# Optimization experiments

Hardware: AMD Instinct MI355X
Metric: run time of the kernel (lower is better)

The kernel has to match this reference:

```python
import jax, jax.numpy as jnp
import numpy as np

D_MODEL = 256
MLP_DIM = 1024
EPS = 1e-5

def _layernorm(x, g, b):
    mu = jnp.mean(x, axis=-1, keepdims=True)
    var = jnp.mean(jnp.square(x - mu), axis=-1, keepdims=True)
    return (x - mu) * jax.lax.rsqrt(var + EPS) * g + b

def setup_inputs() -> dict:
    key = jax.random.key(0)
    ks = jax.random.split(key, 4)
    d, m = D_MODEL, MLP_DIM
    x = jax.random.normal(ks[0], (8, 1024, 4, d), dtype=jnp.float32)
    w_qkv = jax.random.normal(ks[1], (3 * d, d), dtype=jnp.float32) * 0.05  # torch Linear weight (out,in)
    gamma1 = jnp.ones((d,), jnp.float32)
    beta1 = jnp.zeros((d,), jnp.float32)
    gamma2 = jnp.ones((d,), jnp.float32)
    beta2 = jnp.zeros((d,), jnp.float32)
    w1 = jax.random.normal(ks[2], (m, d), dtype=jnp.float32) * 0.05
    b1 = jnp.zeros((m,), jnp.float32)
    w2 = jax.random.normal(ks[3], (d, m), dtype=jnp.float32) * 0.05
    b2 = jnp.zeros((d,), jnp.float32)
    return {"x": x, "w_qkv": w_qkv, "gamma1": gamma1, "beta1": beta1,
            "gamma2": gamma2, "beta2": beta2, "w1": w1, "b1": b1, "w2": w2, "b2": b2}

def reference(x, w_qkv, gamma1, beta1, gamma2, beta2, w1, b1, w2, b2):
    bsz, n, h, d = x.shape
    scale = d ** -0.5
    # --- attention branch: x + attn(norm1(x)) ---
    xn = _layernorm(x, gamma1, beta1)
    # Linear(d, 3d): xn @ W^T, then reshape trailing 3d -> (d, 3) as in torch
    qkv = jnp.einsum('bnhd,ed->bnhe', xn, w_qkv).reshape(bsz, n * h, d, 3)
    q, k, v = qkv[..., 0], qkv[..., 1], qkv[..., 2]   # [b, n*h, d]
    dots = jnp.einsum('bid,bjd->bij', q, k) * scale   # [b, n*h, n*h]
    attn = jax.nn.softmax(dots, axis=-1)              # dropout=0 -> identity
    out = jnp.einsum('bij,bjd->bid', attn, v).reshape(bsz, n, h, d)
    x = x + out
    # --- mlp branch: x + mlp(norm2(x)) ---
    xn2 = _layernorm(x, gamma2, beta2)
    hid = jax.nn.silu(jnp.einsum('bnhd,md->bnhm', xn2, w1) + b1)
    x = x + jnp.einsum('bnhm,dm->bnhd', hid, w2) + b2
    return x
```

## Files before the change

kernel.cpp:

```cpp
#include <hip/hip_runtime.h>


typedef __attribute__((ext_vector_type(8))) short bf16x8;
typedef __attribute__((ext_vector_type(4))) short bf16x4;
typedef __attribute__((ext_vector_type(4))) float f32x4;
typedef __attribute__((ext_vector_type(16))) float f32x16;

static __device__ __forceinline__ short f2bf(float f) {
    union { float f; unsigned u; } v; v.f = f;
    unsigned r = (v.u + 0x7FFFu + ((v.u >> 16) & 1u)) >> 16;
    return (short)r;
}

static __device__ __forceinline__ void gll16(const void* g, void* l) {
    __builtin_amdgcn_global_load_lds(
        (const __attribute__((address_space(1))) unsigned*)g,
        (__attribute__((address_space(3))) unsigned*)l, 16, 0, 0);
}

__global__ __launch_bounds__(256) void k_cvt(const float* __restrict__ wqkv,
                                             const float* __restrict__ w1,
                                             const float* __restrict__ w2,
                                             short* __restrict__ owqkv,
                                             short* __restrict__ ow1,
                                             short* __restrict__ ow2) {
    int i = blockIdx.x * 256 + threadIdx.x;
    if (i < 196608) {
        int e = i >> 8, col = i & 255;
        int dd = e / 3, which = e - dd * 3;
        float v = wqkv[i];
        if (which == 0) v *= 0.0625f * 1.44269504f;
        owqkv[((which << 8) + dd) * 256 + col] = f2bf(v);
    }
    if (i < 262144) { ow1[i] = f2bf(w1[i]); ow2[i] = f2bf(w2[i]); }
}

__global__ __launch_bounds__(256) void k_ln(const float* __restrict__ x,
                                            const float* __restrict__ g,
                                            const float* __restrict__ bta,
                                            short* __restrict__ out) {
    int w = threadIdx.x >> 6, lane = threadIdx.x & 63;
    long row = (long)blockIdx.x * 4 + w;
    float4 v = *((const float4*)(x + row * 256) + lane);
    float s = v.x + v.y + v.z + v.w;
    float q = v.x * v.x + v.y * v.y + v.z * v.z + v.w * v.w;
    for (int off = 1; off < 64; off <<= 1) {
        s += __shfl_xor(s, off);
        q += __shfl_xor(q, off);
    }
    float mean = s * (1.0f / 256.0f);
    float var = q * (1.0f / 256.0f) - mean * mean;
    float rstd = rsqrtf(var + 1e-5f);
    float4 gg = *((const float4*)g + lane);
    float4 bb = *((const float4*)bta + lane);
    short4 o;
    o.x = f2bf((v.x - mean) * rstd * gg.x + bb.x);
    o.y = f2bf((v.y - mean) * rstd * gg.y + bb.y);
    o.z = f2bf((v.z - mean) * rstd * gg.z + bb.z);
    o.w = f2bf((v.w - mean) * rstd * gg.w + bb.w);
    *((short4*)(out + row * 256) + lane) = o;
}

__global__ __launch_bounds__(256) void k_qkv(const short* __restrict__ xn,
                                             const short* __restrict__ wb,
                                             short* __restrict__ Q,
                                             short* __restrict__ K,
                                             short* __restrict__ VT) {
    __shared__ __attribute__((aligned(16))) short lds_a[64 * 264];
    __shared__ __attribute__((aligned(16))) short lds_b[64 * 264];
    int t = threadIdx.x;
    int m0 = blockIdx.y * 64, n0 = blockIdx.x * 64;
    const int4* ga = (const int4*)xn;
    const int4* gb = (const int4*)wb;
    int4* la = (int4*)lds_a;
    int4* lb = (int4*)lds_b;
    for (int it = 0; it < 8; it++) {
        int c = t + 256 * it;
        int r = c >> 5, k = c & 31;
        la[r * 33 + k] = ga[(long)(m0 + r) * 32 + k];
        lb[r * 33 + k] = gb[(n0 + r) * 32 + k];
    }
    __syncthreads();
    int w = t >> 6, lane = t & 63, ln = lane & 15, qd = lane >> 4;
    int moff = (w >> 1) * 32, noff = (w & 1) * 32;
    f32x4 acc[2][2] = {};
    for (int ks = 0; ks < 8; ks++) {
        bf16x8 a0 = *(const bf16x8*)&lds_a[(moff + ln) * 264 + ks * 32 + qd * 8];
        bf16x8 a1 = *(const bf16x8*)&lds_a[(moff + 16 + ln) * 264 + ks * 32 + qd * 8];
        bf16x8 b0 = *(const bf16x8*)&lds_b[(noff + ln) * 264 + ks * 32 + qd * 8];
        bf16x8 b1 = *(const bf16x8*)&lds_b[(noff + 16 + ln) * 264 + ks * 32 + qd * 8];
        acc[0][0] = __builtin_amdgcn_mfma_f32_16x16x32_bf16(a0, b0, acc[0][0], 0, 0, 0);
        acc[0][1] = __builtin_amdgcn_mfma_f32_16x16x32_bf16(a0, b1, acc[0][1], 0, 0, 0);
        acc[1][0] = __builtin_amdgcn_mfma_f32_16x16x32_bf16(a1, b0, acc[1][0], 0, 0, 0);
        acc[1][1] = __builtin_amdgcn_mfma_f32_16x16x32_bf16(a1, b1, acc[1][1], 0, 0, 0);
    }
    for (int mi = 0; mi < 2; mi++)
        for (int nj = 0; nj < 2; nj++)
            for (int rg = 0; rg < 4; rg++) {
                float v = acc[mi][nj][rg];
                int gr = m0 + moff + mi * 16 + qd * 4 + rg;
                int e = n0 + noff + nj * 16 + ln;
                int which = e >> 8, dd = e & 255;
                short bv = f2bf(v);
                if (which == 0) Q[(long)gr * 256 + dd] = bv;
                else if (which == 1) K[(long)gr * 256 + dd] = bv;
                else {
                    int b = gr >> 12, i = gr & 4095;
                    VT[((long)b * 256 + dd) * 4096 + i] = bv;
                }
            }
}

__global__ __launch_bounds__(512, 2) void k_attn(const short* __restrict__ Q,
                                                 const short* __restrict__ K,
                                                 const short* __restrict__ VT,
                                                 const float* __restrict__ x,
                                                 float* __restrict__ out) {
    __shared__ __attribute__((aligned(16))) short lds_k[2][64 * 256];
    __shared__ __attribute__((aligned(16))) short lds_v[2][2][256 * 40];
    int t = threadIdx.x, w = t >> 6, l = t & 63, l5 = l & 31, h = l >> 5;
    int ww = w & 3, hkv = w >> 2;
    int b = blockIdx.x;
    int q0 = blockIdx.y * 128 + ww * 32;

    bf16x8 qf[16];
    {
        const short* qrow = Q + ((long)(b * 4096 + q0 + l5)) * 256;
        #pragma unroll
        for (int kc = 0; kc < 16; kc++) qf[kc] = *(const bf16x8*)(qrow + kc * 16 + h * 8);
    }
    f32x16 O[8] = {};
    float lsum = 0.f;

    const char* Kb = (const char*)(K + (long)b * 4096 * 256);
    const int4* gv = (const int4*)(VT + (long)b * 4096 * 256);

    int koff[4], klds[4];
    #pragma unroll
    for (int i = 0; i < 4; i++) {
        int r = w * 8 + i * 2 + (l >> 5);
        koff[i] = r * 512 + ((l5 ^ (r & 31)) * 16);
        klds[i] = (w * 8 + i * 2) * 512;
    }
    int vgbase[4], vloff[4];
    #pragma unroll
    for (int i = 0; i < 4; i++) {
        int c = t + 512 * i;
        int sub = c >> 10, cc = c & 1023, d = cc >> 2, ch = cc & 3;
        vgbase[i] = d * 512 + sub * 4 + ch;
        vloff[i] = sub * 20480 + d * 80 + ch * 16;
    }
    int4 vs[4];

    #pragma unroll
    for (int i = 0; i < 4; i++) vs[i] = gv[vgbase[i]];
    #pragma unroll
    for (int i = 0; i < 4; i++) gll16(Kb + koff[i], (char*)lds_k[0] + klds[i]);
    #pragma unroll
    for (int i = 0; i < 4; i++)
        *(int4*)((char*)lds_v + vloff[i]) = vs[i];
    __syncthreads();

    const char* lvmine = (const char*)lds_v + hkv * 20480;

    for (int jt = 0; jt < 64; jt++) {
        int cur = jt & 1;
        if (jt < 63) {
            #pragma unroll
            for (int i = 0; i < 4; i++) vs[i] = gv[vgbase[i] + (jt + 1) * 8];
            int ka = (jt + 1) * 32768;
            #pragma unroll
            for (int i = 0; i < 4; i++)
                gll16(Kb + ka + koff[i], (char*)lds_k[cur ^ 1] + klds[i]);
        }
        const short* lk = lds_k[cur] + hkv * 32 * 256;
        const char* lv = lvmine + cur * 40960;
        f32x16 st = {};
        #pragma unroll
        for (int kc = 0; kc < 16; kc++) {
            int cc = kc * 2 + h;
            bf16x8 a = *(const bf16x8*)(lk + (l5 * 32 + (cc ^ l5)) * 8);
            st = __builtin_amdgcn_mfma_f32_32x32x16_bf16(a, qf[kc], st, 0, 0, 0);
        }
        unsigned pw[4][2];
        #pragma unroll
        for (int r4 = 0; r4 < 4; r4++) {
            float p0 = __builtin_amdgcn_exp2f(st[r4 * 4 + 0]);
            float p1 = __builtin_amdgcn_exp2f(st[r4 * 4 + 1]);
            float p2 = __builtin_amdgcn_exp2f(st[r4 * 4 + 2]);
            float p3 = __builtin_amdgcn_exp2f(st[r4 * 4 + 3]);
            lsum += (p0 + p1) + (p2 + p3);
            union { float f; unsigned u; } u0, u1, u2, u3;
            u0.f = p0; u1.f = p1; u2.f = p2; u3.f = p3;
            pw[r4][0] = __builtin_amdgcn_perm(u1.u + 0x8000u, u0.u + 0x8000u, 0x07060302u);
            pw[r4][1] = __builtin_amdgcn_perm(u3.u + 0x8000u, u2.u + 0x8000u, 0x07060302u);
        }
        bf16x8 pfr[2];
        #pragma unroll
        for (int k2 = 0; k2 < 2; k2++) {
            unsigned a0 = pw[2 * k2][0], a1 = pw[2 * k2][1];
            unsigned b0 = pw[2 * k2 + 1][0], b1 = pw[2 * k2 + 1][1];
            asm("v_permlane32_swap_b32 %0, %1" : "+v"(a0), "+v"(b0));
            asm("v_permlane32_swap_b32 %0, %1" : "+v"(a1), "+v"(b1));
            union { unsigned u[4]; bf16x8 v; } f;
            f.u[0] = a0; f.u[1] = a1; f.u[2] = b0; f.u[3] = b1;
            pfr[k2] = f.v;
        }
        if (jt < 63) {
            #pragma unroll
            for (int i = 0; i < 4; i++)
                *(int4*)((char*)lds_v + (cur ^ 1) * 40960 + vloff[i]) = vs[i];
        }
        #pragma unroll
        for (int dt = 0; dt < 8; dt++) {
            const char* vbase = lv + (dt * 32 + l5) * 80;
            #pragma unroll
            for (int k2 = 0; k2 < 2; k2++) {
                bf16x8 va = *(const bf16x8*)(vbase + (k2 * 2 + h) * 16);
                O[dt] = __builtin_amdgcn_mfma_f32_32x32x16_bf16(va, pfr[k2], O[dt], 0, 0, 0);
            }
        }
        __syncthreads();
    }

    float lt = lsum + __shfl_xor(lsum, 32);
    float* lmrg = (float*)&lds_v[1][0][0];
    lmrg[hkv * 128 + ww * 32 + l5] = lt;
    __syncthreads();
    float ltot = lmrg[ww * 32 + l5] + lmrg[128 + ww * 32 + l5];
    float rinv = 1.0f / ltot;

    float* omrg = (float*)&lds_v[0][0][0];
    float* fscr = (float*)lds_k[0] + ww * (32 * 33);
    #pragma unroll
    for (int dt = 0; dt < 8; dt++) {
        if (hkv == 1) {
            #pragma unroll
            for (int r = 0; r < 16; r++) omrg[ww * 1024 + r * 64 + l] = O[dt][r];
        }
        __syncthreads();
        if (hkv == 0) {
            #pragma unroll
            for (int r = 0; r < 16; r++) {
                float Om = O[dt][r] + omrg[ww * 1024 + r * 64 + l];
                int drow = (r & 3) + 8 * (r >> 2) + 4 * h;
                fscr[drow * 33 + l5] = Om * rinv;
            }
            asm volatile("s_waitcnt lgkmcnt(0)" ::: "memory");
            #pragma unroll
            for (int it = 0; it < 16; it++) {
                int ql = it * 2 + h;
                float v = fscr[l5 * 33 + ql];
                long idx = ((long)(b * 4096 + q0 + ql)) * 256 + dt * 32 + l5;
                out[idx] = x[idx] + v;
            }
            asm volatile("s_waitcnt lgkmcnt(0)" ::: "memory");
        }
        __syncthreads();
    }
}

__global__ __launch_bounds__(256) void k_mlp(const short* __restrict__ xn,
                                             const short* __restrict__ w1b,
                                             const short* __restrict__ w2b,
                                             const float* __restrict__ b1,
                                             const float* __restrict__ b2,
                                             float* __restrict__ out) {
    __shared__ __attribute__((aligned(16))) short lds_w[2][32 * 256];
    __shared__ __attribute__((aligned(16))) short lds_h[4][16 * 264];
    int t = threadIdx.x, w = t >> 6, l = t & 63, l5 = l & 31, ln = l & 15, qd = l >> 4;
    int R0 = blockIdx.x * 64 + w * 16;
    short* lhs = lds_h[w];

    bf16x8 a1f[8];
    #pragma unroll
    for (int kc = 0; kc < 8; kc++)
        a1f[kc] = *(const bf16x8*)(xn + (long)(R0 + ln) * 256 + kc * 32 + qd * 8);

    long s1off[4], s2off[4]; int wlds[4];
    #pragma unroll
    for (int i = 0; i < 4; i++) {
        int r = w * 8 + i * 2 + (l >> 5);
        int ch = l5 ^ (r & 31);
        s1off[i] = (long)r * 512 + ch * 16;
        s2off[i] = (long)r * 2048 + ch * 16;
        wlds[i] = (w * 8 + i * 2) * 512;
    }
    const char* W1c = (const char*)w1b;
    const char* W2c = (const char*)w2b;

    f32x4 Oc[8][2] = {};
    #pragma unroll
    for (int i = 0; i < 4; i++)
        gll16(W1c + s1off[i], (char*)lds_w[0] + wlds[i]);
    __syncthreads();
    int cur = 0;

    for (int pass = 0; pass < 4; pass++) {
        #pragma unroll
        for (int nt = 0; nt < 8; nt++) {
            if (nt < 7) {
                long base = (long)(pass * 256 + (nt + 1) * 32) * 512;
                #pragma unroll
                for (int i = 0; i < 4; i++)
                    gll16(W1c + base + s1off[i], (char*)lds_w[cur ^ 1] + wlds[i]);
            } else {
                long base = (long)pass * 512;
                #pragma unroll
                for (int i = 0; i < 4; i++)
                    gll16(W2c + base + s2off[i], (char*)lds_w[cur ^ 1] + wlds[i]);
            }
            const short* lw = lds_w[cur];
            #pragma unroll
            for (int g = 0; g < 2; g++) {
                int lr = g * 16 + ln;
                f32x4 acc = {};
                #pragma unroll
                for (int kc = 0; kc < 8; kc++) {
                    int cc = kc * 4 + qd;
                    bf16x8 bf = *(const bf16x8*)(lw + lr * 256 + (cc ^ lr) * 8);
                    acc = __builtin_amdgcn_mfma_f32_16x16x32_bf16(a1f[kc], bf, acc, 0, 0, 0);
                }
                float bb = b1[pass * 256 + nt * 32 + lr];
                #pragma unroll
                for (int rg = 0; rg < 4; rg++) {
                    float z = acc[rg] + bb;
                    float sv = z / (1.0f + __expf(-z));
                    lhs[(qd * 4 + rg) * 264 + nt * 32 + lr] = f2bf(sv);
                }
            }
            __syncthreads();
            cur ^= 1;
        }
        bf16x8 a2f[8];
        #pragma unroll
        for (int kc = 0; kc < 8; kc++)
            a2f[kc] = *(const bf16x8*)&lhs[ln * 264 + kc * 32 + qd * 8];
        #pragma unroll
        for (int nt = 0; nt < 8; nt++) {
            if (nt < 7) {
                long base = (long)((nt + 1) * 32) * 2048 + (long)pass * 512;
                #pragma unroll
                for (int i = 0; i < 4; i++)
                    gll16(W2c + base + s2off[i], (char*)lds_w[cur ^ 1] + wlds[i]);
            } else if (pass < 3) {
                long base = (long)((pass + 1) * 256) * 512;
                #pragma unroll
                for (int i = 0; i < 4; i++)
                    gll16(W1c + base + s1off[i], (char*)lds_w[cur ^ 1] + wlds[i]);
            }
            const short* lw = lds_w[cur];
            #pragma unroll
            for (int g = 0; g < 2; g++) {
                int lr = g * 16 + ln;
                #pragma unroll
                for (int kc = 0; kc < 8; kc++) {
                    int cc = kc * 4 + qd;
                    bf16x8 bf = *(const bf16x8*)(lw + lr * 256 + (cc ^ lr) * 8);
                    Oc[nt][g] = __builtin_amdgcn_mfma_f32_16x16x32_bf16(a2f[kc], bf, Oc[nt][g], 0, 0, 0);
                }
            }
            __syncthreads();
            cur ^= 1;
        }
    }
    #pragma unroll
    for (int nt = 0; nt < 8; nt++)
        #pragma unroll
        for (int g = 0; g < 2; g++) {
            int dd = nt * 32 + g * 16 + ln;
            float bb = b2[dd];
            #pragma unroll
            for (int rg = 0; rg < 4; rg++) {
                long idx = (long)(R0 + qd * 4 + rg) * 256 + dd;
                out[idx] = out[idx] + Oc[nt][g][rg] + bb;
            }
        }
}

extern "C" void kernel_launch(void* const* d_in, const int* in_sizes, int n_in,
                              void* d_out, int out_size, void* d_ws, size_t ws_size,
                              hipStream_t stream) {
    const float* x    = (const float*)d_in[0];
    const float* wqkv = (const float*)d_in[1];
    const float* g1   = (const float*)d_in[2];
    const float* be1  = (const float*)d_in[3];
    const float* g2   = (const float*)d_in[4];
    const float* be2  = (const float*)d_in[5];
    const float* w1   = (const float*)d_in[6];
    const float* b1   = (const float*)d_in[7];
    const float* w2   = (const float*)d_in[8];
    const float* b2   = (const float*)d_in[9];
    float* out = (float*)d_out;
    char* ws = (char*)d_ws;
    short* WQKV = (short*)(ws);
    short* W1B  = (short*)(ws + (512l << 10));
    short* W2B  = (short*)(ws + (1l << 20));
    short* XN   = (short*)(ws + (2l << 20));
    short* Qb   = (short*)(ws + (18l << 20));
    short* Kb   = (short*)(ws + (34l << 20));
    short* VTb  = (short*)(ws + (50l << 20));

    k_cvt<<<1024, 256, 0, stream>>>(wqkv, w1, w2, WQKV, W1B, W2B);
    k_ln<<<8192, 256, 0, stream>>>(x, g1, be1, XN);
    k_qkv<<<dim3(12, 512), 256, 0, stream>>>(XN, WQKV, Qb, Kb, VTb);
    k_attn<<<dim3(8, 32), 512, 0, stream>>>(Qb, Kb, VTb, x, out);
    k_ln<<<8192, 256, 0, stream>>>(out, g2, be2, XN);
    k_mlp<<<512, 256, 0, stream>>>(XN, W1B, W2B, b1, b2, out);
}
```

Measured before the change: 410.7 us.

## Use async LDS loads in QKV GEMM, coalesce V^T stores, widen MLP blocks

The QKV projection kernel now loads its tiles with global_load_lds into an XOR-swizzled layout instead of padded register-staged copies. V-transpose outputs are staged in LDS and written as 16-byte coalesced rows, replacing scattered 2-byte strided stores. The MLP kernel moves to 512-thread blocks covering 128 rows, so each streamed weight tile is shared by twice as many rows and each thread issues half as many loads. The trade-offs are larger blocks, fewer of them, and an extra LDS round-trip in the V path.

```diff
diff --git a/kernel.cpp b/kernel.cpp
--- a/kernel.cpp
+++ b/kernel.cpp
@@ -66,49 +66,73 @@
                                              short* __restrict__ Q,
                                              short* __restrict__ K,
                                              short* __restrict__ VT) {
-    __shared__ __attribute__((aligned(16))) short lds_a[64 * 264];
-    __shared__ __attribute__((aligned(16))) short lds_b[64 * 264];
-    int t = threadIdx.x;
+    __shared__ __attribute__((aligned(16))) short lds_a[64 * 256];
+    __shared__ __attribute__((aligned(16))) short lds_b[64 * 256];
+    int t = threadIdx.x, w = t >> 6, l = t & 63, l5 = l & 31;
     int m0 = blockIdx.y * 64, n0 = blockIdx.x * 64;
-    const int4* ga = (const int4*)xn;
-    const int4* gb = (const int4*)wb;
-    int4* la = (int4*)lds_a;
-    int4* lb = (int4*)lds_b;
-    for (int it = 0; it < 8; it++) {
-        int c = t + 256 * it;
-        int r = c >> 5, k = c & 31;
-        la[r * 33 + k] = ga[(long)(m0 + r) * 32 + k];
-        lb[r * 33 + k] = gb[(n0 + r) * 32 + k];
+    const char* ga = (const char*)xn + (long)m0 * 512;
+    const char* gb = (const char*)wb + (long)n0 * 512;
+    #pragma unroll
+    for (int i = 0; i < 8; i++) {
+        int r = w * 16 + i * 2 + (l >> 5);
+        int off = r * 512 + ((l5 ^ (r & 31)) * 16);
+        int ldst = (w * 16 + i * 2) * 512;
+        gll16(ga + off, (char*)lds_a + ldst);
+        gll16(gb + off, (char*)lds_b + ldst);
     }
     __syncthreads();
-    int w = t >> 6, lane = t & 63, ln = lane & 15, qd = lane >> 4;
+    int ln = l & 15, qd = l >> 4;
     int moff = (w >> 1) * 32, noff = (w & 1) * 32;
     f32x4 acc[2][2] = {};
+    #pragma unroll
     for (int ks = 0; ks < 8; ks++) {
-        bf16x8 a0 = *(const bf16x8*)&lds_a[(moff + ln) * 264 + ks * 32 + qd * 8];
-        bf16x8 a1 = *(const bf16x8*)&lds_a[(moff + 16 + ln) * 264 + ks * 32 + qd * 8];
-        bf16x8 b0 = *(const bf16x8*)&lds_b[(noff + ln) * 264 + ks * 32 + qd * 8];
-        bf16x8 b1 = *(const bf16x8*)&lds_b[(noff + 16 + ln) * 264 + ks * 32 + qd * 8];
+        int ca = ks * 4 + qd;
+        int ra0 = moff + ln, ra1 = moff + 16 + ln;
+        int rb0 = noff + ln, rb1 = noff + 16 + ln;
+        bf16x8 a0 = *(const bf16x8*)((const char*)lds_a + ra0 * 512 + ((ca ^ (ra0 & 31)) * 16));
+        bf16x8 a1 = *(const bf16x8*)((const char*)lds_a + ra1 * 512 + ((ca ^ (ra1 & 31)) * 16));
+        bf16x8 b0 = *(const bf16x8*)((const char*)lds_b + rb0 * 512 + ((ca ^ (rb0 & 31)) * 16));
+        bf16x8 b1 = *(const bf16x8*)((const char*)lds_b + rb1 * 512 + ((ca ^ (rb1 & 31)) * 16));
         acc[0][0] = __builtin_amdgcn_mfma_f32_16x16x32_bf16(a0, b0, acc[0][0], 0, 0, 0);
         acc[0][1] = __builtin_amdgcn_mfma_f32_16x16x32_bf16(a0, b1, acc[0][1], 0, 0, 0);
         acc[1][0] = __builtin_amdgcn_mfma_f32_16x16x32_bf16(a1, b0, acc[1][0], 0, 0, 0);
         acc[1][1] = __builtin_amdgcn_mfma_f32_16x16x32_bf16(a1, b1, acc[1][1], 0, 0, 0);
     }
-    for (int mi = 0; mi < 2; mi++)
-        for (int nj = 0; nj < 2; nj++)
-            for (int rg = 0; rg < 4; rg++) {
-                float v = acc[mi][nj][rg];
-                int gr = m0 + moff + mi * 16 + qd * 4 + rg;
-                int e = n0 + noff + nj * 16 + ln;
-                int which = e >> 8, dd = e & 255;
-                short bv = f2bf(v);
-                if (which == 0) Q[(long)gr * 256 + dd] = bv;
-                else if (which == 1) K[(long)gr * 256 + dd] = bv;
-                else {
-                    int b = gr >> 12, i = gr & 4095;
-                    VT[((long)b * 256 + dd) * 4096 + i] = bv;
+    if (blockIdx.x < 8) {
+        #pragma unroll
+        for (int mi = 0; mi < 2; mi++)
+            #pragma unroll
+            for (int nj = 0; nj < 2; nj++)
+                #pragma unroll
+                for (int rg = 0; rg < 4; rg++) {
+                    int gr = m0 + moff + mi * 16 + qd * 4 + rg;
+                    int e = n0 + noff + nj * 16 + ln;
+                    short bv = f2bf(acc[mi][nj][rg]);
+                    if (e < 256) Q[(long)gr * 256 + e] = bv;
+                    else K[(long)gr * 256 + (e - 256)] = bv;
                 }
-            }
+    } else {
+        __syncthreads();
+        short* scr = lds_a;
+        #pragma unroll
+        for (int mi = 0; mi < 2; mi++)
+            #pragma unroll
+            for (int nj = 0; nj < 2; nj++)
+                #pragma unroll
+                for (int rg = 0; rg < 4; rg++) {
+                    int dl = noff + nj * 16 + ln;
+                    int il = moff + mi * 16 + qd * 4 + rg;
+                    scr[dl * 88 + il] = f2bf(acc[mi][nj][rg]);
+                }
+        __syncthreads();
+        int bb = m0 >> 12, i0 = m0 & 4095;
+        int dl = t >> 2, ch = t & 3;
+        const int4* s4 = (const int4*)(scr + dl * 88 + ch * 16);
+        int4 v0 = s4[0], v1 = s4[1];
+        long vrow = ((long)(bb * 256 + (n0 - 512) + dl)) * 4096 + i0 + ch * 16;
+        *(int4*)(VT + vrow) = v0;
+        *(int4*)(VT + vrow + 8) = v1;
+    }
 }
 
 __global__ __launch_bounds__(512, 2) void k_attn(const short* __restrict__ Q,
@@ -260,16 +284,16 @@
     }
 }
 
-__global__ __launch_bounds__(256) void k_mlp(const short* __restrict__ xn,
-                                             const short* __restrict__ w1b,
-                                             const short* __restrict__ w2b,
-                                             const float* __restrict__ b1,
-                                             const float* __restrict__ b2,
-                                             float* __restrict__ out) {
+__global__ __launch_bounds__(512, 2) void k_mlp(const short* __restrict__ xn,
+                                                const short* __restrict__ w1b,
+                                                const short* __restrict__ w2b,
+                                                const float* __restrict__ b1,
+                                                const float* __restrict__ b2,
+                                                float* __restrict__ out) {
     __shared__ __attribute__((aligned(16))) short lds_w[2][32 * 256];
-    __shared__ __attribute__((aligned(16))) short lds_h[4][16 * 264];
+    __shared__ __attribute__((aligned(16))) short lds_h[8][16 * 264];
     int t = threadIdx.x, w = t >> 6, l = t & 63, l5 = l & 31, ln = l & 15, qd = l >> 4;
-    int R0 = blockIdx.x * 64 + w * 16;
+    int R0 = blockIdx.x * 128 + w * 16;
     short* lhs = lds_h[w];
 
     bf16x8 a1f[8];
@@ -277,21 +301,21 @@
     for (int kc = 0; kc < 8; kc++)
         a1f[kc] = *(const bf16x8*)(xn + (long)(R0 + ln) * 256 + kc * 32 + qd * 8);
 
-    long s1off[4], s2off[4]; int wlds[4];
-    #pragma unroll
-    for (int i = 0; i < 4; i++) {
-        int r = w * 8 + i * 2 + (l >> 5);
+    long s1off[2], s2off[2]; int wlds[2];
+    #pragma unroll
+    for (int i = 0; i < 2; i++) {
+        int r = w * 4 + i * 2 + (l >> 5);
         int ch = l5 ^ (r & 31);
         s1off[i] = (long)r * 512 + ch * 16;
         s2off[i] = (long)r * 2048 + ch * 16;
-        wlds[i] = (w * 8 + i * 2) * 512;
+        wlds[i] = (w * 4 + i * 2) * 512;
     }
     const char* W1c = (const char*)w1b;
     const char* W2c = (const char*)w2b;
 
     f32x4 Oc[8][2] = {};
     #pragma unroll
-    for (int i = 0; i < 4; i++)
+    for (int i = 0; i < 2; i++)
         gll16(W1c + s1off[i], (char*)lds_w[0] + wlds[i]);
     __syncthreads();
     int cur = 0;
@@ -302,12 +326,12 @@
             if (nt < 7) {
                 long base = (long)(pass * 256 + (nt + 1) * 32) * 512;
                 #pragma unroll
-                for (int i = 0; i < 4; i++)
+                for (int i = 0; i < 2; i++)
                     gll16(W1c + base + s1off[i], (char*)lds_w[cur ^ 1] + wlds[i]);
             } else {
                 long base = (long)pass * 512;
                 #pragma unroll
-                for (int i = 0; i < 4; i++)
+                for (int i = 0; i < 2; i++)
                     gll16(W2c + base + s2off[i], (char*)lds_w[cur ^ 1] + wlds[i]);
             }
             const short* lw = lds_w[cur];
@@ -341,12 +365,12 @@
             if (nt < 7) {
                 long base = (long)((nt + 1) * 32) * 2048 + (long)pass * 512;
                 #pragma unroll
-                for (int i = 0; i < 4; i++)
+                for (int i = 0; i < 2; i++)
                     gll16(W2c + base + s2off[i], (char*)lds_w[cur ^ 1] + wlds[i]);
             } else if (pass < 3) {
                 long base = (long)((pass + 1) * 256) * 512;
                 #pragma unroll
-                for (int i = 0; i < 4; i++)
+                for (int i = 0; i < 2; i++)
                     gll16(W1c + base + s1off[i], (char*)lds_w[cur ^ 1] + wlds[i]);
             }
             const short* lw = lds_w[cur];
@@ -406,5 +430,5 @@
     k_qkv<<<dim3(12, 512), 256, 0, stream>>>(XN, WQKV, Qb, Kb, VTb);
     k_attn<<<dim3(8, 32), 512, 0, stream>>>(Qb, Kb, VTb, x, out);
     k_ln<<<8192, 256, 0, stream>>>(out, g2, be2, XN);
-    k_mlp<<<512, 256, 0, stream>>>(XN, W1B, W2B, b1, b2, out);
-}
+    k_mlp<<<256, 512, 0, stream>>>(XN, W1B, W2B, b1, b2, out);
+}
```

Result: no change. 410.1 us (-0.2%).
